# Kernel optimization log

Measured on AMD Instinct MI355X. Metric: run time of the kernel, lower is better.

The kernel has to match this reference:

```python
import jax, jax.numpy as jnp
import numpy as np

B, S, HID = 2, 2048, 2048
NH, HD, G = 16, 128, 4
NKV = NH // G  # 4
ROPE_THETA = 10000.0


def _xavier(key, shape):
    fan_in, fan_out = shape
    lim = float(np.sqrt(6.0 / (fan_in + fan_out)))
    return jax.random.uniform(key, shape, jnp.float32, -lim, lim)


def setup_inputs() -> dict:
    key = jax.random.key(0)
    ks = jax.random.split(key, 6)
    hidden_states = jax.random.normal(ks[0], (B, S, HID), jnp.float32)
    # mask==True means MASKED (code adds mask * -1e9): causal upper triangle
    causal = jnp.triu(jnp.ones((S, S), jnp.bool_), k=1)
    mask = jnp.broadcast_to(causal[None, None], (B, 1, S, S))
    return {
        "hidden_states": hidden_states,
        "mask": mask,
        "Wq": _xavier(ks[1], (HID, NH * HD)),
        "bq": jnp.zeros((NH * HD,), jnp.float32),
        "Wk": _xavier(ks[2], (HID, NKV * HD)),
        "bk": jnp.zeros((NKV * HD,), jnp.float32),
        "Wv": _xavier(ks[3], (HID, NKV * HD)),
        "bv": jnp.zeros((NKV * HD,), jnp.float32),
        "Wo": _xavier(ks[4], (NH * HD, HID)),
        "bo": jnp.zeros((HID,), jnp.float32),
    }


def _rope_cos_sin(seq_len, head_dim, dtype):
    half = head_dim // 2
    inv_freq = 1.0 / (ROPE_THETA ** (jnp.arange(0, half, dtype=jnp.float32) / half))
    ang = jnp.arange(seq_len, dtype=jnp.float32)[:, None] * inv_freq[None, :]  # [S, half]
    # shape [1, S, 1, half] for broadcasting over (B, S, H, half)
    return jnp.cos(ang)[None, :, None, :].astype(dtype), jnp.sin(ang)[None, :, None, :].astype(dtype)


def _apply_rope(x, cos, sin):
    half = x.shape[-1] // 2
    x1, x2 = x[..., :half], x[..., half:]
    return jnp.concatenate([x1 * cos - x2 * sin, x1 * sin + x2 * cos], axis=-1)


def reference(hidden_states, mask, Wq, bq, Wk, bk, Wv, bv, Wo, bo):
    b, s, _ = hidden_states.shape
    scale = 1.0 / jnp.sqrt(jnp.asarray(HD, hidden_states.dtype))

    q = (hidden_states @ Wq + bq).reshape(b, s, NH, HD)
    k = (hidden_states @ Wk + bk).reshape(b, s, NKV, HD)
    v = (hidden_states @ Wv + bv).reshape(b, s, NKV, HD)

    cos, sin = _rope_cos_sin(s, HD, hidden_states.dtype)
    q = _apply_rope(q, cos, sin)
    k = _apply_rope(k, cos, sin)

    q = jnp.transpose(q, (0, 2, 1, 3))          # [B, NH, S, D]
    k = jnp.transpose(k, (0, 2, 1, 3))          # [B, NKV, S, D]
    v = jnp.transpose(v, (0, 2, 1, 3))          # [B, NKV, S, D]

    # GQA: group query heads instead of repeating K/V (same math as jnp.repeat)
    qg = q.reshape(b, NKV, G, s, HD)
    scores = jnp.einsum('bngqd,bnkd->bngqk', qg, k) * scale  # [B, NKV, G, S, S]

    maskf = mask.astype(scores.dtype)[:, :, None]  # [B, 1, 1, S, S]
    scores = scores + maskf * (-1e9)

    probs = jax.nn.softmax(scores, axis=-1)
    out = jnp.einsum('bngqk,bnkd->bngqd', probs, v)          # [B, NKV, G, S, D]
    out = out.reshape(b, NH, s, HD).transpose(0, 2, 1, 3).reshape(b, s, NH * HD)
    return out @ Wo + bo
```

## Files before the change

kernel.cpp:

```cpp
#include <hip/hip_runtime.h>
#include <hip/hip_bf16.h>

#define B_ 2
#define S_ 2048
#define HID_ 2048
#define NH_ 16
#define HD_ 128
#define NKV_ 4
#define M_ (B_*S_)
#define NQKV_ 3072
#define QSCALE 0.08838834764831845f

typedef __bf16 bf16x8 __attribute__((ext_vector_type(8)));
typedef float f32x4 __attribute__((ext_vector_type(4)));
typedef float f32x16 __attribute__((ext_vector_type(16)));

typedef __attribute__((address_space(1))) const unsigned int gas_uint;
typedef __attribute__((address_space(3))) unsigned int las_uint;

__device__ __forceinline__ unsigned short f2bfu(float x) {
  __hip_bfloat16 h = __float2bfloat16(x);
  return __builtin_bit_cast(unsigned short, h);
}

__device__ __forceinline__ unsigned int pack2bf(float lo, float hi) {
  return (unsigned int)f2bfu(lo) | ((unsigned int)f2bfu(hi) << 16);
}

__device__ __forceinline__ void gload_lds16(const void* g, void* l) {
  __builtin_amdgcn_global_load_lds((gas_uint*)g, (las_uint*)l, 16, 0, 0);
}


__global__ void k_cvt(const float* __restrict__ src, unsigned short* __restrict__ dst, int n4) {
  int i = blockIdx.x * 256 + threadIdx.x;
  if (i >= n4) return;
  float4 v = ((const float4*)src)[i];
  ushort4 o;
  o.x = f2bfu(v.x); o.y = f2bfu(v.y); o.z = f2bfu(v.z); o.w = f2bfu(v.w);
  ((ushort4*)dst)[i] = o;
}

__global__ void k_tcvt(const float* __restrict__ src, unsigned short* __restrict__ dst, int R, int C) {
  __shared__ float t[32][33];
  int bc = blockIdx.x * 32, br = blockIdx.y * 32;
  int tx = threadIdx.x & 31, ty = threadIdx.x >> 5;
  for (int i = ty; i < 32; i += 8)
    t[i][tx] = src[(size_t)(br + i) * C + bc + tx];
  __syncthreads();
  for (int i = ty; i < 32; i += 8)
    dst[(size_t)(bc + i) * R + br + tx] = f2bfu(t[tx][i]);
}

__global__ void k_bias(const float* __restrict__ bq, const float* __restrict__ bk,
                       const float* __restrict__ bv, float* __restrict__ out) {
  int i = blockIdx.x * 256 + threadIdx.x;
  float v = (i < 2048) ? bq[i] : (i < 2560 ? bk[i - 2048] : bv[i - 2560]);
  out[i] = v;
}

__global__ void k_ropetab(float* __restrict__ cosT, float* __restrict__ sinT) {
  int idx = blockIdx.x * 256 + threadIdx.x;
  int s = idx >> 6, i = idx & 63;
  float invf = expf(-(float)i * (9.210340371976184f / 64.f));
  float ang = (float)s * invf;
  cosT[idx] = cosf(ang);
  sinT[idx] = sinf(ang);
}

__global__ void k_ropeq(const float* __restrict__ Cq, const float* __restrict__ cosT,
                        const float* __restrict__ sinT, unsigned short* __restrict__ Qr) {
  int idx = blockIdx.x * 256 + threadIdx.x;
  int i = idx & 63, h = (idx >> 6) & (NH_ - 1), m = idx >> 10;
  int s = m & (S_ - 1), b = m >> 11;
  const float* row = Cq + (size_t)m * NQKV_ + h * HD_;
  float x1 = row[i], x2 = row[i + 64];
  float c = cosT[(s << 6) + i], sn = sinT[(s << 6) + i];
  size_t base = ((size_t)(b * NH_ + h) * S_ + s) * HD_;
  Qr[base + i]      = f2bfu((x1 * c - x2 * sn) * QSCALE);
  Qr[base + i + 64] = f2bfu((x1 * sn + x2 * c) * QSCALE);
}

__global__ void k_ropek(const float* __restrict__ Cq, const float* __restrict__ cosT,
                        const float* __restrict__ sinT, unsigned short* __restrict__ Kr) {
  int idx = blockIdx.x * 256 + threadIdx.x;
  int i = idx & 63, kv = (idx >> 6) & (NKV_ - 1), m = idx >> 8;
  int s = m & (S_ - 1), b = m >> 11;
  const float* row = Cq + (size_t)m * NQKV_ + 2048 + kv * HD_;
  float x1 = row[i], x2 = row[i + 64];
  float c = cosT[(s << 6) + i], sn = sinT[(s << 6) + i];
  size_t base = ((size_t)(b * NKV_ + kv) * S_ + s) * HD_;
  Kr[base + i]      = f2bfu(x1 * c - x2 * sn);
  Kr[base + i + 64] = f2bfu(x1 * sn + x2 * c);
}

__global__ void k_vt(const float* __restrict__ Cq, unsigned short* __restrict__ Vt) {
  __shared__ float t[32][129];
  int bx = blockIdx.x;
  int st = bx & 63, kv = (bx >> 6) & 3, b = bx >> 8;
  int s0 = st * 32;
  int tid = threadIdx.x;
  for (int j = 0; j < 16; ++j) {
    int idx = j * 256 + tid;
    int si = idx >> 7, d = idx & 127;
    t[si][d] = Cq[(size_t)(b * S_ + s0 + si) * NQKV_ + 2560 + kv * HD_ + d];
  }
  __syncthreads();
  for (int j = 0; j < 16; ++j) {
    int idx = j * 256 + tid;
    int d = idx >> 5, si = idx & 31;
    Vt[((size_t)(b * NKV_ + kv) * HD_ + d) * S_ + s0 + si] = f2bfu(t[si][d]);
  }
}


__global__ __launch_bounds__(256, 2)
void k_gemm(const unsigned short* __restrict__ A, const unsigned short* __restrict__ Bt,
            const float* __restrict__ bias, float* __restrict__ C,
            int Md, int Nd, int Kd) {
  __shared__ __align__(16) unsigned short As[128 * 64];
  __shared__ __align__(16) unsigned short Bs[128 * 64];
  int nt = Nd >> 7;
  int nwg = (Md >> 7) * nt;
  int bid = blockIdx.x;
  int wg = bid;
  if ((nwg & 7) == 0) { int cpx = nwg >> 3; wg = (bid & 7) * cpx + (bid >> 3); }
  int bm = wg / nt, bn = wg - bm * nt;
  int tid = threadIdx.x;
  int lane = tid & 63, w = tid >> 6;
  int wm = (w >> 1) << 6, wn = (w & 1) << 6;
  int lr = lane & 15, lg = lane >> 4;
  f32x4 acc[4][4] = {};

  const int chunkbase = w << 2;
  const int boff = lane << 4;
  const int nK = Kd >> 6;
  const size_t rowstride = (size_t)Kd * 2;

  for (int kt = 0; kt < nK; ++kt) {
#pragma unroll
    for (int i = 0; i < 4; ++i) {
      int off = ((chunkbase + i) << 10) + boff;
      int row = off >> 7;
      int colb = off & 127;
      int scolb = colb ^ ((row & 7) << 4);
      const char* ga = (const char*)A + (size_t)(bm * 128 + row) * rowstride + (kt << 7) + scolb;
      const char* gb = (const char*)Bt + (size_t)(bn * 128 + row) * rowstride + (kt << 7) + scolb;
      gload_lds16(ga, (char*)As + ((chunkbase + i) << 10));
      gload_lds16(gb, (char*)Bs + ((chunkbase + i) << 10));
    }
    __syncthreads();
#pragma unroll
    for (int kk = 0; kk < 2; ++kk) {
      bf16x8 a[4], b[4];
      int kb = ((kk << 5) + (lg << 3)) << 1;
#pragma unroll
      for (int mi = 0; mi < 4; ++mi) {
        int row = wm + (mi << 4) + lr;
        a[mi] = *(const bf16x8*)((const char*)As + (row << 7) + (kb ^ ((row & 7) << 4)));
      }
#pragma unroll
      for (int ni = 0; ni < 4; ++ni) {
        int row = wn + (ni << 4) + lr;
        b[ni] = *(const bf16x8*)((const char*)Bs + (row << 7) + (kb ^ ((row & 7) << 4)));
      }
#pragma unroll
      for (int mi = 0; mi < 4; ++mi)
#pragma unroll
        for (int ni = 0; ni < 4; ++ni)
          acc[mi][ni] = __builtin_amdgcn_mfma_f32_16x16x32_bf16(a[mi], b[ni], acc[mi][ni], 0, 0, 0);
    }
    __syncthreads();
  }
#pragma unroll
  for (int mi = 0; mi < 4; ++mi) {
    int r0 = bm * 128 + wm + (mi << 4) + (lg << 2);
#pragma unroll
    for (int ni = 0; ni < 4; ++ni) {
      int col = bn * 128 + wn + (ni << 4) + lr;
      float bz = bias[col];
#pragma unroll
      for (int r = 0; r < 4; ++r)
        C[(size_t)(r0 + r) * Nd + col] = acc[mi][ni][r] + bz;
    }
  }
}


__global__ __launch_bounds__(256, 2)
void k_attn(const unsigned short* __restrict__ Qr, const unsigned short* __restrict__ Kr,
            const unsigned short* __restrict__ Vt, unsigned short* __restrict__ Ob) {
  __shared__ __align__(16) unsigned short Ks[2][64 * 128];
  int bid = blockIdx.x;
  int bx = (bid & 7) * 64 + (bid >> 3);
  int qt = 15 - (bx & 15);
  int h = (bx >> 4) & 15, b = bx >> 8;
  int kvh = h >> 2;
  int tid = threadIdx.x, lane = tid & 63, w = tid >> 6;
  int ql = lane & 31, hi = lane >> 5;
  int q0 = (qt << 7) + (w << 5);
  int qrow = q0 + ql;

  const unsigned short* Qp = Qr + (((size_t)(b * NH_ + h) * S_) << 7);
  const unsigned short* Kp = Kr + (((size_t)(b * NKV_ + kvh) * S_) << 7);
  const unsigned short* Vp = Vt + (((size_t)(b * NKV_ + kvh) * HD_) << 11);

  bf16x8 qa[8];
#pragma unroll
  for (int c = 0; c < 8; ++c)
    qa[c] = *(const bf16x8*)(Qp + (((size_t)qrow) << 7) + (c << 4) + (hi << 3));

  f32x16 acc[4] = {};
  float m_r = -1e30f, l_r = 0.f;

  const int ntile = (qt + 1) << 1;

#define STAGE_K(bsel, t)                                                        \
  {                                                                             \
    const char* kbase = (const char*)Kp + ((size_t)(t) << 14);                  \
    _Pragma("unroll")                                                           \
    for (int i_ = 0; i_ < 4; ++i_) {                                            \
      int woff_ = (i_ << 12) + (w << 10);                                       \
      int off_ = woff_ + (lane << 4);                                           \
      int row_ = off_ >> 8;                                                     \
      int colb_ = off_ & 255;                                                   \
      int scolb_ = colb_ ^ ((row_ & 15) << 4);                                  \
      gload_lds16(kbase + ((size_t)row_ << 8) + scolb_,                         \
                  (char*)Ks[bsel] + woff_);                                     \
    }                                                                           \
  }

  STAGE_K(0, 0);
  __syncthreads();

  for (int t = 0; t < ntile; ++t) {
    if (t + 1 < ntile) STAGE_K((t + 1) & 1, t + 1);
    const char* Kb = (const char*)Ks[t & 1];

#pragma unroll
    for (int sub = 0; sub < 2; ++sub) {
      int kvbase = (t << 6) + (sub << 5);
      if (kvbase > q0 + 31) continue;

      f32x16 st = {};
      int krow = (sub << 5) + ql;
      int sw = (krow & 15) << 4;
#pragma unroll
      for (int c = 0; c < 8; ++c) {
        int cb = (c << 5) + (hi << 4);
        bf16x8 kf = *(const bf16x8*)(Kb + (krow << 8) + (cb ^ sw));
        st = __builtin_amdgcn_mfma_f32_32x32x16_bf16(kf, qa[c], st, 0, 0, 0);
      }
      if (kvbase + 31 > q0) {
#pragma unroll
        for (int r = 0; r < 16; ++r) {
          int kv = kvbase + (r & 3) + ((r >> 2) << 3) + (hi << 2);
          if (kv > qrow) st[r] = -1e30f;
        }
      }
      float pmax = st[0];
#pragma unroll
      for (int r = 1; r < 16; ++r) pmax = fmaxf(pmax, st[r]);
      pmax = fmaxf(pmax, __shfl_xor(pmax, 32));
      if (!__all(pmax <= m_r + 8.f)) {
        float mn = fmaxf(m_r, pmax);
        float al = __expf(m_r - mn);
        m_r = mn;
        l_r *= al;
#pragma unroll
        for (int dc = 0; dc < 4; ++dc) acc[dc] = acc[dc] * al;
      }
      float p[16];
      float ps = 0.f;
#pragma unroll
      for (int r = 0; r < 16; ++r) { p[r] = __expf(st[r] - m_r); ps += p[r]; }
      ps += __shfl_xor(ps, 32);
      l_r += ps;
      unsigned int W[8];
#pragma unroll
      for (int i = 0; i < 8; ++i) W[i] = pack2bf(p[2 * i], p[2 * i + 1]);
      unsigned int pw0 = __shfl_xor(W[0], 32), pw1 = __shfl_xor(W[1], 32);
      unsigned int pw2 = __shfl_xor(W[2], 32), pw3 = __shfl_xor(W[3], 32);
      unsigned int pw4 = __shfl_xor(W[4], 32), pw5 = __shfl_xor(W[5], 32);
      unsigned int pw6 = __shfl_xor(W[6], 32), pw7 = __shfl_xor(W[7], 32);
      uint4 u0, u1;
      u0.x = hi ? pw2 : W[0];
      u0.y = hi ? pw3 : W[1];
      u0.z = hi ? W[2] : pw0;
      u0.w = hi ? W[3] : pw1;
      u1.x = hi ? pw6 : W[4];
      u1.y = hi ? pw7 : W[5];
      u1.z = hi ? W[6] : pw4;
      u1.w = hi ? W[7] : pw5;
      bf16x8 pa0 = __builtin_bit_cast(bf16x8, u0);
      bf16x8 pa1 = __builtin_bit_cast(bf16x8, u1);
#pragma unroll
      for (int dc = 0; dc < 4; ++dc) {
        const unsigned short* vrow = Vp + (((size_t)((dc << 5) + ql)) << 11) + kvbase + (hi << 3);
        bf16x8 vf0 = *(const bf16x8*)(vrow);
        bf16x8 vf1 = *(const bf16x8*)(vrow + 16);
        acc[dc] = __builtin_amdgcn_mfma_f32_32x32x16_bf16(vf0, pa0, acc[dc], 0, 0, 0);
        acc[dc] = __builtin_amdgcn_mfma_f32_32x32x16_bf16(vf1, pa1, acc[dc], 0, 0, 0);
      }
    }
    __syncthreads();
  }

  float inv = 1.f / l_r;
  unsigned short* obase = Ob + ((((size_t)(b * S_) + qrow)) << 11) + (h << 7) + (hi << 2);
#pragma unroll
  for (int dc = 0; dc < 4; ++dc)
#pragma unroll
    for (int g = 0; g < 4; ++g) {
      ushort4 o;
      o.x = f2bfu(acc[dc][4 * g + 0] * inv);
      o.y = f2bfu(acc[dc][4 * g + 1] * inv);
      o.z = f2bfu(acc[dc][4 * g + 2] * inv);
      o.w = f2bfu(acc[dc][4 * g + 3] * inv);
      *(ushort4*)(obase + (dc << 5) + (g << 3)) = o;
    }
}


extern "C" void kernel_launch(void* const* d_in, const int* in_sizes, int n_in,
                              void* d_out, int out_size, void* d_ws, size_t ws_size,
                              hipStream_t stream) {
  const float* X  = (const float*)d_in[0];
  const float* Wq = (const float*)d_in[2];
  const float* bq = (const float*)d_in[3];
  const float* Wk = (const float*)d_in[4];
  const float* bk = (const float*)d_in[5];
  const float* Wv = (const float*)d_in[6];
  const float* bv = (const float*)d_in[7];
  const float* Wo = (const float*)d_in[8];
  const float* bo = (const float*)d_in[9];
  float* out = (float*)d_out;

  char* ws = (char*)d_ws;
  unsigned short* Xb  = (unsigned short*)(ws);
  unsigned short* Wt  = (unsigned short*)(ws + 16777216);
  unsigned short* Wot = (unsigned short*)(ws + 29360128);
  float* Bqkv         = (float*)(ws + 37748736);
  float* cosT         = (float*)(ws + 37761024);
  float* sinT         = (float*)(ws + 38285312);
  float* Cqkv         = (float*)(ws + 38809600);
  unsigned short* Qr  = (unsigned short*)(ws + 89141248);
  unsigned short* Kr  = (unsigned short*)(ws + 105918464);
  unsigned short* Vtb = (unsigned short*)(ws + 110112768);
  unsigned short* Ob  = (unsigned short*)(ws + 114307072);

  k_cvt<<<(M_ * HID_ / 4 + 255) / 256, 256, 0, stream>>>(X, Xb, M_ * HID_ / 4);
  k_tcvt<<<dim3(2048 / 32, 2048 / 32), 256, 0, stream>>>(Wq, Wt, 2048, 2048);
  k_tcvt<<<dim3(512 / 32, 2048 / 32), 256, 0, stream>>>(Wk, Wt + 2048 * 2048, 2048, 512);
  k_tcvt<<<dim3(512 / 32, 2048 / 32), 256, 0, stream>>>(Wv, Wt + 2560 * 2048, 2048, 512);
  k_tcvt<<<dim3(2048 / 32, 2048 / 32), 256, 0, stream>>>(Wo, Wot, 2048, 2048);
  k_bias<<<12, 256, 0, stream>>>(bq, bk, bv, Bqkv);
  k_ropetab<<<S_ * 64 / 256, 256, 0, stream>>>(cosT, sinT);

  k_gemm<<<(M_ / 128) * (NQKV_ / 128), 256, 0, stream>>>(Xb, Wt, Bqkv, Cqkv, M_, NQKV_, HID_);

  k_ropeq<<<M_ * NH_ * 64 / 256, 256, 0, stream>>>(Cqkv, cosT, sinT, Qr);
  k_ropek<<<M_ * NKV_ * 64 / 256, 256, 0, stream>>>(Cqkv, cosT, sinT, Kr);
  k_vt<<<B_ * NKV_ * (S_ / 32), 256, 0, stream>>>(Cqkv, Vtb);

  k_attn<<<B_ * NH_ * (S_ / 128), 256, 0, stream>>>(Qr, Kr, Vtb, Ob);

  k_gemm<<<(M_ / 128) * (HID_ / 128), 256, 0, stream>>>(Ob, Wot, bo, out, M_, HID_, NH_ * HD_);
}
```

Before: 277.6 us.

## Run attention as single-wave blocks reading K directly from global memory

Replaces the 4-wave attention block that double-buffers K tiles in shared memory with one-wave blocks, each handling 32 query rows. K is now loaded straight from global memory (through the caches) with no LDS staging or block barriers. The grid is remapped so the 8 low block-id bits pick batch and KV head, which spreads blocks sharing the same K/V across the device for L2 locality. The aim is to remove barrier stalls, balance work across blocks more finely, and raise occupancy, at the cost of losing K reuse in LDS across four waves and adding more global memory traffic.

```diff
diff --git a/kernel.cpp b/kernel.cpp
--- a/kernel.cpp
+++ b/kernel.cpp
@@ -187,18 +187,19 @@
 }
 
 
-__global__ __launch_bounds__(256, 2)
+__global__ __launch_bounds__(64)
 void k_attn(const unsigned short* __restrict__ Qr, const unsigned short* __restrict__ Kr,
             const unsigned short* __restrict__ Vt, unsigned short* __restrict__ Ob) {
-  __shared__ __align__(16) unsigned short Ks[2][64 * 128];
   int bid = blockIdx.x;
-  int bx = (bid & 7) * 64 + (bid >> 3);
-  int qt = 15 - (bx & 15);
-  int h = (bx >> 4) & 15, b = bx >> 8;
-  int kvh = h >> 2;
-  int tid = threadIdx.x, lane = tid & 63, w = tid >> 6;
+  int g = bid & 7;
+  int qi2 = bid >> 3;
+  int hg = qi2 >> 6;
+  int qt = 63 - (qi2 & 63);
+  int b = g >> 2, kvh = g & 3;
+  int h = (kvh << 2) + hg;
+  int lane = threadIdx.x & 63;
   int ql = lane & 31, hi = lane >> 5;
-  int q0 = (qt << 7) + (w << 5);
+  int q0 = qt << 5;
   int qrow = q0 + ql;
 
   const unsigned short* Qp = Qr + (((size_t)(b * NH_ + h) * S_) << 7);
@@ -213,97 +214,65 @@
   f32x16 acc[4] = {};
   float m_r = -1e30f, l_r = 0.f;
 
-  const int ntile = (qt + 1) << 1;
-
-#define STAGE_K(bsel, t)                                                        \
-  {                                                                             \
-    const char* kbase = (const char*)Kp + ((size_t)(t) << 14);                  \
-    _Pragma("unroll")                                                           \
-    for (int i_ = 0; i_ < 4; ++i_) {                                            \
-      int woff_ = (i_ << 12) + (w << 10);                                       \
-      int off_ = woff_ + (lane << 4);                                           \
-      int row_ = off_ >> 8;                                                     \
-      int colb_ = off_ & 255;                                                   \
-      int scolb_ = colb_ ^ ((row_ & 15) << 4);                                  \
-      gload_lds16(kbase + ((size_t)row_ << 8) + scolb_,                         \
-                  (char*)Ks[bsel] + woff_);                                     \
-    }                                                                           \
-  }
-
-  STAGE_K(0, 0);
-  __syncthreads();
-
-  for (int t = 0; t < ntile; ++t) {
-    if (t + 1 < ntile) STAGE_K((t + 1) & 1, t + 1);
-    const char* Kb = (const char*)Ks[t & 1];
-
-#pragma unroll
-    for (int sub = 0; sub < 2; ++sub) {
-      int kvbase = (t << 6) + (sub << 5);
-      if (kvbase > q0 + 31) continue;
-
-      f32x16 st = {};
-      int krow = (sub << 5) + ql;
-      int sw = (krow & 15) << 4;
-#pragma unroll
-      for (int c = 0; c < 8; ++c) {
-        int cb = (c << 5) + (hi << 4);
-        bf16x8 kf = *(const bf16x8*)(Kb + (krow << 8) + (cb ^ sw));
-        st = __builtin_amdgcn_mfma_f32_32x32x16_bf16(kf, qa[c], st, 0, 0, 0);
+  for (int kvbase = 0; kvbase <= q0; kvbase += 32) {
+    const unsigned short* krow_p = Kp + ((size_t)(kvbase + ql) << 7) + (hi << 3);
+    f32x16 st = {};
+#pragma unroll
+    for (int c = 0; c < 8; ++c) {
+      bf16x8 kf = *(const bf16x8*)(krow_p + (c << 4));
+      st = __builtin_amdgcn_mfma_f32_32x32x16_bf16(kf, qa[c], st, 0, 0, 0);
+    }
+    if (kvbase == q0) {
+#pragma unroll
+      for (int r = 0; r < 16; ++r) {
+        int kv = kvbase + (r & 3) + ((r >> 2) << 3) + (hi << 2);
+        if (kv > qrow) st[r] = -1e30f;
       }
-      if (kvbase + 31 > q0) {
-#pragma unroll
-        for (int r = 0; r < 16; ++r) {
-          int kv = kvbase + (r & 3) + ((r >> 2) << 3) + (hi << 2);
-          if (kv > qrow) st[r] = -1e30f;
-        }
-      }
-      float pmax = st[0];
-#pragma unroll
-      for (int r = 1; r < 16; ++r) pmax = fmaxf(pmax, st[r]);
-      pmax = fmaxf(pmax, __shfl_xor(pmax, 32));
-      if (!__all(pmax <= m_r + 8.f)) {
-        float mn = fmaxf(m_r, pmax);
-        float al = __expf(m_r - mn);
-        m_r = mn;
-        l_r *= al;
-#pragma unroll
-        for (int dc = 0; dc < 4; ++dc) acc[dc] = acc[dc] * al;
-      }
-      float p[16];
-      float ps = 0.f;
-#pragma unroll
-      for (int r = 0; r < 16; ++r) { p[r] = __expf(st[r] - m_r); ps += p[r]; }
-      ps += __shfl_xor(ps, 32);
-      l_r += ps;
-      unsigned int W[8];
-#pragma unroll
-      for (int i = 0; i < 8; ++i) W[i] = pack2bf(p[2 * i], p[2 * i + 1]);
-      unsigned int pw0 = __shfl_xor(W[0], 32), pw1 = __shfl_xor(W[1], 32);
-      unsigned int pw2 = __shfl_xor(W[2], 32), pw3 = __shfl_xor(W[3], 32);
-      unsigned int pw4 = __shfl_xor(W[4], 32), pw5 = __shfl_xor(W[5], 32);
-      unsigned int pw6 = __shfl_xor(W[6], 32), pw7 = __shfl_xor(W[7], 32);
-      uint4 u0, u1;
-      u0.x = hi ? pw2 : W[0];
-      u0.y = hi ? pw3 : W[1];
-      u0.z = hi ? W[2] : pw0;
-      u0.w = hi ? W[3] : pw1;
-      u1.x = hi ? pw6 : W[4];
-      u1.y = hi ? pw7 : W[5];
-      u1.z = hi ? W[6] : pw4;
-      u1.w = hi ? W[7] : pw5;
-      bf16x8 pa0 = __builtin_bit_cast(bf16x8, u0);
-      bf16x8 pa1 = __builtin_bit_cast(bf16x8, u1);
-#pragma unroll
-      for (int dc = 0; dc < 4; ++dc) {
-        const unsigned short* vrow = Vp + (((size_t)((dc << 5) + ql)) << 11) + kvbase + (hi << 3);
-        bf16x8 vf0 = *(const bf16x8*)(vrow);
-        bf16x8 vf1 = *(const bf16x8*)(vrow + 16);
-        acc[dc] = __builtin_amdgcn_mfma_f32_32x32x16_bf16(vf0, pa0, acc[dc], 0, 0, 0);
-        acc[dc] = __builtin_amdgcn_mfma_f32_32x32x16_bf16(vf1, pa1, acc[dc], 0, 0, 0);
-      }
-    }
-    __syncthreads();
+    }
+    float pmax = st[0];
+#pragma unroll
+    for (int r = 1; r < 16; ++r) pmax = fmaxf(pmax, st[r]);
+    pmax = fmaxf(pmax, __shfl_xor(pmax, 32));
+    if (!__all(pmax <= m_r + 8.f)) {
+      float mn = fmaxf(m_r, pmax);
+      float al = __expf(m_r - mn);
+      m_r = mn;
+      l_r *= al;
+#pragma unroll
+      for (int dc = 0; dc < 4; ++dc) acc[dc] = acc[dc] * al;
+    }
+    float p[16];
+    float ps = 0.f;
+#pragma unroll
+    for (int r = 0; r < 16; ++r) { p[r] = __expf(st[r] - m_r); ps += p[r]; }
+    ps += __shfl_xor(ps, 32);
+    l_r += ps;
+    unsigned int W[8];
+#pragma unroll
+    for (int i = 0; i < 8; ++i) W[i] = pack2bf(p[2 * i], p[2 * i + 1]);
+    unsigned int pw0 = __shfl_xor(W[0], 32), pw1 = __shfl_xor(W[1], 32);
+    unsigned int pw2 = __shfl_xor(W[2], 32), pw3 = __shfl_xor(W[3], 32);
+    unsigned int pw4 = __shfl_xor(W[4], 32), pw5 = __shfl_xor(W[5], 32);
+    unsigned int pw6 = __shfl_xor(W[6], 32), pw7 = __shfl_xor(W[7], 32);
+    uint4 u0, u1;
+    u0.x = hi ? pw2 : W[0];
+    u0.y = hi ? pw3 : W[1];
+    u0.z = hi ? W[2] : pw0;
+    u0.w = hi ? W[3] : pw1;
+    u1.x = hi ? pw6 : W[4];
+    u1.y = hi ? pw7 : W[5];
+    u1.z = hi ? W[6] : pw4;
+    u1.w = hi ? W[7] : pw5;
+    bf16x8 pa0 = __builtin_bit_cast(bf16x8, u0);
+    bf16x8 pa1 = __builtin_bit_cast(bf16x8, u1);
+#pragma unroll
+    for (int dc = 0; dc < 4; ++dc) {
+      const unsigned short* vrow = Vp + (((size_t)((dc << 5) + ql)) << 11) + kvbase + (hi << 3);
+      bf16x8 vf0 = *(const bf16x8*)(vrow);
+      bf16x8 vf1 = *(const bf16x8*)(vrow + 16);
+      acc[dc] = __builtin_amdgcn_mfma_f32_32x32x16_bf16(vf0, pa0, acc[dc], 0, 0, 0);
+      acc[dc] = __builtin_amdgcn_mfma_f32_32x32x16_bf16(vf1, pa1, acc[dc], 0, 0, 0);
+    }
   }
 
   float inv = 1.f / l_r;
@@ -311,13 +280,13 @@
 #pragma unroll
   for (int dc = 0; dc < 4; ++dc)
 #pragma unroll
-    for (int g = 0; g < 4; ++g) {
+    for (int gq = 0; gq < 4; ++gq) {
       ushort4 o;
-      o.x = f2bfu(acc[dc][4 * g + 0] * inv);
-      o.y = f2bfu(acc[dc][4 * g + 1] * inv);
-      o.z = f2bfu(acc[dc][4 * g + 2] * inv);
-      o.w = f2bfu(acc[dc][4 * g + 3] * inv);
-      *(ushort4*)(obase + (dc << 5) + (g << 3)) = o;
+      o.x = f2bfu(acc[dc][4 * gq + 0] * inv);
+      o.y = f2bfu(acc[dc][4 * gq + 1] * inv);
+      o.z = f2bfu(acc[dc][4 * gq + 2] * inv);
+      o.w = f2bfu(acc[dc][4 * gq + 3] * inv);
+      *(ushort4*)(obase + (dc << 5) + (gq << 3)) = o;
     }
 }
 
@@ -363,7 +332,7 @@
   k_ropek<<<M_ * NKV_ * 64 / 256, 256, 0, stream>>>(Cqkv, cosT, sinT, Kr);
   k_vt<<<B_ * NKV_ * (S_ / 32), 256, 0, stream>>>(Cqkv, Vtb);
 
-  k_attn<<<B_ * NH_ * (S_ / 128), 256, 0, stream>>>(Qr, Kr, Vtb, Ob);
+  k_attn<<<B_ * NH_ * (S_ / 32), 64, 0, stream>>>(Qr, Kr, Vtb, Ob);
 
   k_gemm<<<(M_ / 128) * (HID_ / 128), 256, 0, stream>>>(Ob, Wot, bo, out, M_, HID_, NH_ * HD_);
 }
```

After: 316.7 us. 14.1% more time.

## Split attention KV range across two blocks and merge partials in combine kernel

Applied to the files above, without the earlier changes.

Each (batch, head, query-tile) now runs as two blocks that process interleaved 64-wide KV tiles (even or odd). Each block writes a normalized bf16 partial output plus its row max and sum, and a new combine kernel merges the two with log-sum-exp weights. The aim is to double the number of attention blocks and balance the causal workload so the GPU is better occupied. As a smaller change, Q is pre-scaled by log2(e) so softmax can use exp2f, and the deferred-rescale threshold is adjusted to match. The cost is an extra kernel launch, extra partial-output traffic through workspace that reuses the Cqkv buffer, and an additional bf16 rounding step on the partials.

```diff
diff --git a/kernel.cpp b/kernel.cpp
--- a/kernel.cpp
+++ b/kernel.cpp
@@ -9,7 +9,8 @@
 #define NKV_ 4
 #define M_ (B_*S_)
 #define NQKV_ 3072
-#define QSCALE 0.08838834764831845f
+#define QSCALE2 0.12752464484148957f
+#define DEFER_THR 11.5425f
 
 typedef __bf16 bf16x8 __attribute__((ext_vector_type(8)));
 typedef float f32x4 __attribute__((ext_vector_type(4)));
@@ -25,6 +26,13 @@
 
 __device__ __forceinline__ unsigned int pack2bf(float lo, float hi) {
   return (unsigned int)f2bfu(lo) | ((unsigned int)f2bfu(hi) << 16);
+}
+
+__device__ __forceinline__ float bflo(unsigned int u) {
+  return __builtin_bit_cast(float, u << 16);
+}
+__device__ __forceinline__ float bfhi(unsigned int u) {
+  return __builtin_bit_cast(float, u & 0xffff0000u);
 }
 
 __device__ __forceinline__ void gload_lds16(const void* g, void* l) {
@@ -77,8 +85,8 @@
   float x1 = row[i], x2 = row[i + 64];
   float c = cosT[(s << 6) + i], sn = sinT[(s << 6) + i];
   size_t base = ((size_t)(b * NH_ + h) * S_ + s) * HD_;
-  Qr[base + i]      = f2bfu((x1 * c - x2 * sn) * QSCALE);
-  Qr[base + i + 64] = f2bfu((x1 * sn + x2 * c) * QSCALE);
+  Qr[base + i]      = f2bfu((x1 * c - x2 * sn) * QSCALE2);
+  Qr[base + i + 64] = f2bfu((x1 * sn + x2 * c) * QSCALE2);
 }
 
 __global__ void k_ropek(const float* __restrict__ Cq, const float* __restrict__ cosT,
@@ -189,13 +197,19 @@
 
 __global__ __launch_bounds__(256, 2)
 void k_attn(const unsigned short* __restrict__ Qr, const unsigned short* __restrict__ Kr,
-            const unsigned short* __restrict__ Vt, unsigned short* __restrict__ Ob) {
+            const unsigned short* __restrict__ Vt,
+            unsigned short* __restrict__ Po0, unsigned short* __restrict__ Po1,
+            float2* __restrict__ Ml0, float2* __restrict__ Ml1) {
   __shared__ __align__(16) unsigned short Ks[2][64 * 128];
   int bid = blockIdx.x;
-  int bx = (bid & 7) * 64 + (bid >> 3);
-  int qt = 15 - (bx & 15);
-  int h = (bx >> 4) & 15, b = bx >> 8;
-  int kvh = h >> 2;
+  int g = bid & 7;
+  int b = g >> 2, kvh = g & 3;
+  int r = bid >> 3;
+  int split = r & 1;
+  int r2 = r >> 1;
+  int hg = r2 >> 4;
+  int qt = 15 - (r2 & 15);
+  int h = (kvh << 2) + hg;
   int tid = threadIdx.x, lane = tid & 63, w = tid >> 6;
   int ql = lane & 31, hi = lane >> 5;
   int q0 = (qt << 7) + (w << 5);
@@ -213,7 +227,7 @@
   f32x16 acc[4] = {};
   float m_r = -1e30f, l_r = 0.f;
 
-  const int ntile = (qt + 1) << 1;
+  const int nit = qt + 1;
 
 #define STAGE_K(bsel, t)                                                        \
   {                                                                             \
@@ -230,12 +244,13 @@
     }                                                                           \
   }
 
-  STAGE_K(0, 0);
+  STAGE_K(0, split);
   __syncthreads();
 
-  for (int t = 0; t < ntile; ++t) {
-    if (t + 1 < ntile) STAGE_K((t + 1) & 1, t + 1);
-    const char* Kb = (const char*)Ks[t & 1];
+  for (int i = 0; i < nit; ++i) {
+    int t = split + (i << 1);
+    if (i + 1 < nit) STAGE_K((i + 1) & 1, t + 2);
+    const char* Kb = (const char*)Ks[i & 1];
 
 #pragma unroll
     for (int sub = 0; sub < 2; ++sub) {
@@ -253,18 +268,18 @@
       }
       if (kvbase + 31 > q0) {
 #pragma unroll
-        for (int r = 0; r < 16; ++r) {
-          int kv = kvbase + (r & 3) + ((r >> 2) << 3) + (hi << 2);
-          if (kv > qrow) st[r] = -1e30f;
+        for (int rr = 0; rr < 16; ++rr) {
+          int kv = kvbase + (rr & 3) + ((rr >> 2) << 3) + (hi << 2);
+          if (kv > qrow) st[rr] = -1e30f;
         }
       }
       float pmax = st[0];
 #pragma unroll
-      for (int r = 1; r < 16; ++r) pmax = fmaxf(pmax, st[r]);
+      for (int rr = 1; rr < 16; ++rr) pmax = fmaxf(pmax, st[rr]);
       pmax = fmaxf(pmax, __shfl_xor(pmax, 32));
-      if (!__all(pmax <= m_r + 8.f)) {
+      if (!__all(pmax <= m_r + DEFER_THR)) {
         float mn = fmaxf(m_r, pmax);
-        float al = __expf(m_r - mn);
+        float al = exp2f(m_r - mn);
         m_r = mn;
         l_r *= al;
 #pragma unroll
@@ -273,12 +288,12 @@
       float p[16];
       float ps = 0.f;
 #pragma unroll
-      for (int r = 0; r < 16; ++r) { p[r] = __expf(st[r] - m_r); ps += p[r]; }
+      for (int rr = 0; rr < 16; ++rr) { p[rr] = exp2f(st[rr] - m_r); ps += p[rr]; }
       ps += __shfl_xor(ps, 32);
       l_r += ps;
       unsigned int W[8];
 #pragma unroll
-      for (int i = 0; i < 8; ++i) W[i] = pack2bf(p[2 * i], p[2 * i + 1]);
+      for (int i2 = 0; i2 < 8; ++i2) W[i2] = pack2bf(p[2 * i2], p[2 * i2 + 1]);
       unsigned int pw0 = __shfl_xor(W[0], 32), pw1 = __shfl_xor(W[1], 32);
       unsigned int pw2 = __shfl_xor(W[2], 32), pw3 = __shfl_xor(W[3], 32);
       unsigned int pw4 = __shfl_xor(W[4], 32), pw5 = __shfl_xor(W[5], 32);
@@ -306,19 +321,45 @@
     __syncthreads();
   }
 
-  float inv = 1.f / l_r;
-  unsigned short* obase = Ob + ((((size_t)(b * S_) + qrow)) << 11) + (h << 7) + (hi << 2);
+  unsigned short* Pob = split ? Po1 : Po0;
+  float2* Mlb = split ? Ml1 : Ml0;
+  float inv = (l_r > 0.f) ? (1.f / l_r) : 0.f;
+  unsigned short* obase = Pob + ((((size_t)(b * S_) + qrow)) << 11) + (h << 7) + (hi << 2);
 #pragma unroll
   for (int dc = 0; dc < 4; ++dc)
 #pragma unroll
-    for (int g = 0; g < 4; ++g) {
+    for (int gq = 0; gq < 4; ++gq) {
       ushort4 o;
-      o.x = f2bfu(acc[dc][4 * g + 0] * inv);
-      o.y = f2bfu(acc[dc][4 * g + 1] * inv);
-      o.z = f2bfu(acc[dc][4 * g + 2] * inv);
-      o.w = f2bfu(acc[dc][4 * g + 3] * inv);
-      *(ushort4*)(obase + (dc << 5) + (g << 3)) = o;
+      o.x = f2bfu(acc[dc][4 * gq + 0] * inv);
+      o.y = f2bfu(acc[dc][4 * gq + 1] * inv);
+      o.z = f2bfu(acc[dc][4 * gq + 2] * inv);
+      o.w = f2bfu(acc[dc][4 * gq + 3] * inv);
+      *(ushort4*)(obase + (dc << 5) + (gq << 3)) = o;
     }
+  if (hi == 0)
+    Mlb[((size_t)(b * S_) + qrow) * NH_ + h] = make_float2(m_r, l_r);
+}
+
+__global__ void k_comb(const unsigned short* __restrict__ Po0, const unsigned short* __restrict__ Po1,
+                       const float2* __restrict__ Ml0, const float2* __restrict__ Ml1,
+                       unsigned short* __restrict__ Ob) {
+  int idx = blockIdx.x * 256 + threadIdx.x;
+  int c = idx >> 4;
+  float2 a0 = Ml0[c], a1 = Ml1[c];
+  float m = fmaxf(a0.x, a1.x);
+  float w0 = a0.y * exp2f(a0.x - m);
+  float w1 = a1.y * exp2f(a1.x - m);
+  float inv = 1.f / (w0 + w1);
+  w0 *= inv; w1 *= inv;
+  size_t e = (size_t)idx << 3;
+  uint4 v0 = *(const uint4*)(Po0 + e);
+  uint4 v1 = *(const uint4*)(Po1 + e);
+  uint4 o;
+  o.x = pack2bf(w0 * bflo(v0.x) + w1 * bflo(v1.x), w0 * bfhi(v0.x) + w1 * bfhi(v1.x));
+  o.y = pack2bf(w0 * bflo(v0.y) + w1 * bflo(v1.y), w0 * bfhi(v0.y) + w1 * bfhi(v1.y));
+  o.z = pack2bf(w0 * bflo(v0.z) + w1 * bflo(v1.z), w0 * bfhi(v0.z) + w1 * bfhi(v1.z));
+  o.w = pack2bf(w0 * bflo(v0.w) + w1 * bflo(v1.w), w0 * bfhi(v0.w) + w1 * bfhi(v1.w));
+  *(uint4*)(Ob + e) = o;
 }
 
 
@@ -348,6 +389,10 @@
   unsigned short* Kr  = (unsigned short*)(ws + 105918464);
   unsigned short* Vtb = (unsigned short*)(ws + 110112768);
   unsigned short* Ob  = (unsigned short*)(ws + 114307072);
+  unsigned short* Po0 = (unsigned short*)(ws + 38809600);
+  unsigned short* Po1 = (unsigned short*)(ws + 38809600 + 16777216);
+  float2* Ml0         = (float2*)(ws + 38809600 + 33554432);
+  float2* Ml1         = (float2*)(ws + 38809600 + 34078720);
 
   k_cvt<<<(M_ * HID_ / 4 + 255) / 256, 256, 0, stream>>>(X, Xb, M_ * HID_ / 4);
   k_tcvt<<<dim3(2048 / 32, 2048 / 32), 256, 0, stream>>>(Wq, Wt, 2048, 2048);
@@ -363,7 +408,8 @@
   k_ropek<<<M_ * NKV_ * 64 / 256, 256, 0, stream>>>(Cqkv, cosT, sinT, Kr);
   k_vt<<<B_ * NKV_ * (S_ / 32), 256, 0, stream>>>(Cqkv, Vtb);
 
-  k_attn<<<B_ * NH_ * (S_ / 128), 256, 0, stream>>>(Qr, Kr, Vtb, Ob);
+  k_attn<<<B_ * NH_ * (S_ / 128) * 2, 256, 0, stream>>>(Qr, Kr, Vtb, Po0, Po1, Ml0, Ml1);
+  k_comb<<<M_ * HID_ / 8 / 256, 256, 0, stream>>>(Po0, Po1, Ml0, Ml1, Ob);
 
   k_gemm<<<(M_ / 128) * (HID_ / 128), 256, 0, stream>>>(Ob, Wot, bo, out, M_, HID_, NH_ * HD_);
 }
```

New measurement: 260.9 us. -6.0%, faster.
